# Optimization experiments

Hardware: AMD Instinct MI355X
Metric: run time of the kernel (lower is better)

The kernel has to match this reference:

```python
import jax, jax.numpy as jnp
import numpy as np

E, H, I = 5, 768, 1024  # num_experts, hidden_dim, intermediate_dim
TOP_K = 2


def setup_inputs() -> dict:
    key = jax.random.key(0)
    ks = jax.random.split(key, 6)
    s = 0.02
    return {
        "x": jax.random.normal(ks[0], (4, 2048, H), dtype=jnp.float32),
        "router_w": jax.random.normal(ks[1], (E, H), dtype=jnp.float32) * s,  # torch Linear (out,in)
        "router_b": jnp.zeros((E,), dtype=jnp.float32),
        "gate_w": jax.random.normal(ks[2], (E, H, I), dtype=jnp.float32) * s,
        "up_w": jax.random.normal(ks[3], (E, H, I), dtype=jnp.float32) * s,
        "down_w": jax.random.normal(ks[4], (E, I, H), dtype=jnp.float32) * s,
    }


def reference(x, router_w, router_b, gate_w, up_w, down_w):
    B, S, Hd = x.shape
    xf = x.reshape(-1, Hd)                       # [T, H]
    T = xf.shape[0]
    # Router: linear (with bias) -> softmax -> top-2 -> renormalize
    logits = xf @ router_w.T + router_b          # [T, E]
    scores = jax.nn.softmax(logits, axis=-1)
    vals, idx = jax.lax.top_k(scores, TOP_K)     # [T, 2]
    vals = vals / jnp.sum(vals, axis=-1, keepdims=True)
    # Dense combine weights: zero for unselected experts (same math as the
    # per-expert gather/scatter loop in the original module).
    comb = jnp.zeros((T, gate_w.shape[0]), dtype=x.dtype)
    comb = comb.at[jnp.arange(T)[:, None], idx].add(vals)  # [T, E]
    # SwiGLU per expert, vectorized over experts
    g = jnp.einsum('th,ehi->tei', xf, gate_w)    # [T, E, I]
    u = jnp.einsum('th,ehi->tei', xf, up_w)
    y = jnp.einsum('tei,eih->teh', jax.nn.silu(g) * u, down_w)  # [T, E, H]
    out = jnp.einsum('teh,te->th', y, comb)
    return out.reshape(B, S, Hd)
```

## Files before the change

kernel.cpp:

```cpp
#include <hip/hip_runtime.h>
#include <hip/hip_bf16.h>
#include <cstdint>
#include <cstddef>

#define T_TOK 8192
#define H_DIM 768
#define I_DIM 1024
#define N_EXP 5
#define MAXTILE 136

typedef short v8s __attribute__((ext_vector_type(8)));
typedef float v4f __attribute__((ext_vector_type(4)));

static __device__ __forceinline__ unsigned short f2bf(float f) {
    union { float f; unsigned int u; } v; v.f = f;
    unsigned int u = v.u;
    unsigned int r = (u + 0x7fffu + ((u >> 16) & 1u)) >> 16;
    return (unsigned short)r;
}
static __device__ __forceinline__ float bf2f(unsigned short s) {
    union { unsigned int u; float f; } v; v.u = ((unsigned int)s) << 16; return v.f;
}

static __device__ __forceinline__ void async16(const unsigned short* g, unsigned short* l) {
    __builtin_amdgcn_global_load_lds(
        (const __attribute__((address_space(1))) unsigned int*)g,
        (__attribute__((address_space(3))) unsigned int*)l, 16, 0, 0);
}

__global__ void k_prep(const float* __restrict__ gw, const float* __restrict__ uw,
                       const float* __restrict__ dw,
                       unsigned short* __restrict__ wbt, unsigned short* __restrict__ dbt,
                       const float* __restrict__ x, const float* __restrict__ rw,
                       const float* __restrict__ rb, unsigned short* __restrict__ xb,
                       int* __restrict__ top2e, float2* __restrict__ top2w) {
    const int z = blockIdx.z;
    const int tid = threadIdx.x;
    if (z < 3 * N_EXP) {
        __shared__ float tile[32][33];
        const int row = tid >> 3, cq = tid & 7;
        const int ocol = tid >> 3, seg = tid & 7;
        if (z < 2 * N_EXP) {
            if (blockIdx.y >= H_DIM / 32) return;
            const int e = z % N_EXP;
            const int isUp = z >= N_EXP;
            const float* src = (isUp ? uw : gw) + (size_t)e * H_DIM * I_DIM;
            const int c0 = blockIdx.x * 32, r0 = blockIdx.y * 32;
            float4 v = *(const float4*)(src + (size_t)(r0 + row) * I_DIM + c0 + cq * 4);
            tile[row][cq * 4 + 0] = v.x; tile[row][cq * 4 + 1] = v.y;
            tile[row][cq * 4 + 2] = v.z; tile[row][cq * 4 + 3] = v.w;
            __syncthreads();
            int c = c0 + ocol;
            int orow = (c >> 4) * 32 + (c & 15) + (isUp ? 16 : 0);
            ushort4 o;
            o.x = f2bf(tile[seg * 4 + 0][ocol]); o.y = f2bf(tile[seg * 4 + 1][ocol]);
            o.z = f2bf(tile[seg * 4 + 2][ocol]); o.w = f2bf(tile[seg * 4 + 3][ocol]);
            *(ushort4*)(wbt + ((size_t)e * 2 * I_DIM + orow) * H_DIM + r0 + seg * 4) = o;
        } else {
            if (blockIdx.x >= H_DIM / 32) return;
            const int e = z - 2 * N_EXP;
            const float* src = dw + (size_t)e * I_DIM * H_DIM;
            unsigned short* dst = dbt + (size_t)e * I_DIM * H_DIM;
            const int c0 = blockIdx.x * 32, r0 = blockIdx.y * 32;
            float4 v = *(const float4*)(src + (size_t)(r0 + row) * H_DIM + c0 + cq * 4);
            tile[row][cq * 4 + 0] = v.x; tile[row][cq * 4 + 1] = v.y;
            tile[row][cq * 4 + 2] = v.z; tile[row][cq * 4 + 3] = v.w;
            __syncthreads();
            ushort4 o;
            o.x = f2bf(tile[seg * 4 + 0][ocol]); o.y = f2bf(tile[seg * 4 + 1][ocol]);
            o.z = f2bf(tile[seg * 4 + 2][ocol]); o.w = f2bf(tile[seg * 4 + 3][ocol]);
            *(ushort4*)(dst + (size_t)(c0 + ocol) * I_DIM + r0 + seg * 4) = o;
        }
    } else {
        const int wave = tid >> 6, lane = tid & 63;
        const int t = (((z - 3 * N_EXP) * 1024 + blockIdx.y * 32 + blockIdx.x) * 4) + wave;
        const float* xr = x + (size_t)t * H_DIM;
        unsigned short* xbr = xb + (size_t)t * H_DIM;
        float acc[N_EXP];
#pragma unroll
        for (int e = 0; e < N_EXP; e++) acc[e] = 0.f;
#pragma unroll
        for (int j = 0; j < H_DIM / 256; j++) {
            int idx = j * 256 + lane * 4;
            float4 xv = *(const float4*)(xr + idx);
            ushort4 o;
            o.x = f2bf(xv.x); o.y = f2bf(xv.y); o.z = f2bf(xv.z); o.w = f2bf(xv.w);
            *(ushort4*)(xbr + idx) = o;
#pragma unroll
            for (int e = 0; e < N_EXP; e++) {
                float4 wv = *(const float4*)(rw + e * H_DIM + idx);
                acc[e] += xv.x * wv.x + xv.y * wv.y + xv.z * wv.z + xv.w * wv.w;
            }
        }
#pragma unroll
        for (int s = 32; s > 0; s >>= 1) {
#pragma unroll
            for (int e = 0; e < N_EXP; e++) acc[e] += __shfl_down(acc[e], s);
        }
        if (lane == 0) {
            float l[N_EXP];
#pragma unroll
            for (int e = 0; e < N_EXP; e++) l[e] = acc[e] + rb[e];
            int i1 = 0;
#pragma unroll
            for (int e = 1; e < N_EXP; e++) if (l[e] > l[i1]) i1 = e;
            int i2 = (i1 == 0) ? 1 : 0;
#pragma unroll
            for (int e = 0; e < N_EXP; e++) if (e != i1 && l[e] > l[i2]) i2 = e;
            float w1 = 1.f / (1.f + __expf(l[i2] - l[i1]));
            top2e[t] = i1 | (i2 << 8);
            top2w[t] = make_float2(w1, 1.f - w1);
        }
    }
}

__global__ void k_router_b(const int* __restrict__ top2e, const float2* __restrict__ top2w,
                           int* __restrict__ cnt, int* __restrict__ tokslot,
                           float* __restrict__ pweight, int* __restrict__ done,
                           int4* __restrict__ tiles) {
    __shared__ int lcnt[N_EXP], lbase[N_EXP];
    const int tid = threadIdx.x;
    if (tid < N_EXP) lcnt[tid] = 0;
    __syncthreads();
    const int t = blockIdx.x * 256 + tid;
    const int pe = top2e[t];
    const float2 wv = top2w[t];
    const int e1 = pe & 0xff, e2 = pe >> 8;
    const int s1 = atomicAdd(&lcnt[e1], 1);
    const int s2 = atomicAdd(&lcnt[e2], 1);
    __syncthreads();
    if (tid < N_EXP) lbase[tid] = atomicAdd(&cnt[tid], lcnt[tid]);
    __syncthreads();
    const int p1 = lbase[e1] + s1;
    tokslot[e1 * T_TOK + p1] = t; pweight[e1 * T_TOK + p1] = wv.x;
    const int p2 = lbase[e2] + s2;
    tokslot[e2 * T_TOK + p2] = t | (1 << 16); pweight[e2 * T_TOK + p2] = wv.y;
    __syncthreads();
    if (tid == 0) {
        __threadfence();
        if (atomicAdd(done, 1) == (int)gridDim.x - 1) {
            int c[N_EXP], off = 0, idx = 0;
            for (int e = 0; e < N_EXP; e++) c[e] = atomicAdd(&cnt[e], 0);
            for (int e = 0; e < N_EXP; e++) {
                for (int m0 = 0; m0 < c[e]; m0 += 128)
                    tiles[idx++] = make_int4(e, m0, off, c[e]);
                off += c[e];
            }
            for (; idx < MAXTILE; idx++) tiles[idx] = make_int4(-1, 0, 0, 0);
        }
    }
}

__launch_bounds__(256, 4)
__global__ void k_gateup(const unsigned short* __restrict__ xb,
                         const unsigned short* __restrict__ wbt,
                         const int4* __restrict__ tiles,
                         const int* __restrict__ tokslot,
                         const float* __restrict__ pweight,
                         unsigned short* __restrict__ hbuf) {
    const int4 td = tiles[blockIdx.x];
    const int e = td.x;
    if (e < 0) return;
    const int m0 = td.y, offe = td.z, cn = td.w;
    const int n0 = blockIdx.y * 64;

    __shared__ __align__(16) unsigned short ldsA[128 * 64];
    __shared__ __align__(16) unsigned short ldsB[128 * 64];

    const int tid = threadIdx.x;
    const int lane = tid & 63;
    const int wave = tid >> 6;
    const int fm = lane & 15, quad = lane >> 4;

    const int prow = lane >> 3;
    const int pc = lane & 7;
    const int lc8 = (pc ^ prow) * 8;

    unsigned aOff[4];
#pragma unroll
    for (int c = 0; c < 4; c++) {
        const int gr = m0 + c * 32 + wave * 8 + prow;
        const int tk = (gr < cn) ? (tokslot[e * T_TOK + gr] & 0xFFFF) : 0;
        aOff[c] = (unsigned)tk * H_DIM;
    }
    const unsigned short* aBase = xb + lc8;
    const unsigned short* bBase =
        wbt + ((size_t)e * 2 * I_DIM + n0 * 2 + wave * 8 + prow) * H_DIM + lc8;
    unsigned short* ldsAW = ldsA + wave * 8 * 64;
    unsigned short* ldsBW = ldsB + wave * 8 * 64;

    const int wm = (wave & 1) * 64, wnw = wave >> 1;

    v4f acc[4][4];
#pragma unroll
    for (int i = 0; i < 4; i++)
#pragma unroll
        for (int j = 0; j < 4; j++) acc[i][j] = (v4f)0.f;

    for (int kb = 0; kb < H_DIM / 64; kb++) {
        const int k0 = kb * 64;
#pragma unroll
        for (int c = 0; c < 4; c++)
            async16(aBase + aOff[c] + k0, ldsAW + c * 32 * 64);
#pragma unroll
        for (int c = 0; c < 4; c++)
            async16(bBase + (size_t)c * 32 * H_DIM + k0, ldsBW + c * 32 * 64);
        __syncthreads();
#pragma unroll
        for (int ks = 0; ks < 2; ks++) {
            const int pq = ((ks * 4 + quad) ^ (fm & 7)) * 8;
            v8s aF[4], bF[4];
#pragma unroll
            for (int im = 0; im < 4; im++)
                aF[im] = *(const v8s*)&ldsA[(wm + im * 16 + fm) * 64 + pq];
#pragma unroll
            for (int in = 0; in < 4; in++)
                bF[in] = *(const v8s*)&ldsB[(wnw * 64 + in * 16 + fm) * 64 + pq];
#pragma unroll
            for (int im = 0; im < 4; im++)
#pragma unroll
                for (int in = 0; in < 4; in++)
                    acc[im][in] = __builtin_amdgcn_mfma_f32_16x16x32_bf16(aF[im], bF[in], acc[im][in], 0, 0, 0);
        }
        __syncthreads();
    }

#pragma unroll
    for (int im = 0; im < 4; im++) {
        const int lr0 = wm + im * 16 + quad * 4;
        const float4 pw4 = *(const float4*)(pweight + e * T_TOK + m0 + lr0);
#pragma unroll
        for (int reg = 0; reg < 4; reg++) {
            int gr = m0 + lr0 + reg;
            if (gr < cn) {
                float pw = (&pw4.x)[reg];
                size_t base = (size_t)(offe + gr) * I_DIM + n0 + wnw * 32 + fm;
#pragma unroll
                for (int j = 0; j < 2; j++) {
                    float g = acc[im][2 * j][reg];
                    float u = acc[im][2 * j + 1][reg];
                    float s = g / (1.f + __expf(-g));
                    hbuf[base + j * 16] = f2bf(s * u * pw);
                }
            }
        }
    }
}

__launch_bounds__(256, 4)
__global__ void k_down(const unsigned short* __restrict__ hbuf,
                       const unsigned short* __restrict__ dbt,
                       const int4* __restrict__ tiles,
                       const int* __restrict__ tokslot,
                       unsigned short* __restrict__ ybuf) {
    const int4 td = tiles[blockIdx.x];
    const int e = td.x;
    if (e < 0) return;
    const int m0 = td.y, offe = td.z, cn = td.w;
    const int n0 = blockIdx.y * 128;

    __shared__ __align__(16) unsigned short ldsA[128 * 64];
    __shared__ __align__(16) unsigned short ldsB[128 * 64];

    const int tid = threadIdx.x;
    const int lane = tid & 63;
    const int wave = tid >> 6;
    const int fm = lane & 15, quad = lane >> 4;

    const int prow = lane >> 3;
    const int pc = lane & 7;
    const int lc8 = (pc ^ prow) * 8;

    unsigned aOff[4];
#pragma unroll
    for (int c = 0; c < 4; c++) {
        int ar = m0 + c * 32 + wave * 8 + prow;
        if (ar >= cn) ar = cn - 1;
        aOff[c] = (unsigned)(offe + ar) * I_DIM;
    }
    const unsigned short* aBase = hbuf + lc8;
    const unsigned short* bBase =
        dbt + ((size_t)e * H_DIM + n0 + wave * 8 + prow) * I_DIM + lc8;
    unsigned short* ldsAW = ldsA + wave * 8 * 64;
    unsigned short* ldsBW = ldsB + wave * 8 * 64;

    const int wm = (wave & 1) * 64, wn = (wave >> 1) * 64;

    v4f acc[4][4];
#pragma unroll
    for (int i = 0; i < 4; i++)
#pragma unroll
        for (int j = 0; j < 4; j++) acc[i][j] = (v4f)0.f;

    for (int kb = 0; kb < I_DIM / 64; kb++) {
        const int k0 = kb * 64;
#pragma unroll
        for (int c = 0; c < 4; c++)
            async16(aBase + aOff[c] + k0, ldsAW + c * 32 * 64);
#pragma unroll
        for (int c = 0; c < 4; c++)
            async16(bBase + (size_t)c * 32 * I_DIM + k0, ldsBW + c * 32 * 64);
        __syncthreads();
#pragma unroll
        for (int ks = 0; ks < 2; ks++) {
            const int pq = ((ks * 4 + quad) ^ (fm & 7)) * 8;
            v8s aF[4], bF[4];
#pragma unroll
            for (int im = 0; im < 4; im++)
                aF[im] = *(const v8s*)&ldsA[(wm + im * 16 + fm) * 64 + pq];
#pragma unroll
            for (int in = 0; in < 4; in++)
                bF[in] = *(const v8s*)&ldsB[(wn + in * 16 + fm) * 64 + pq];
#pragma unroll
            for (int im = 0; im < 4; im++)
#pragma unroll
                for (int in = 0; in < 4; in++)
                    acc[im][in] = __builtin_amdgcn_mfma_f32_16x16x32_bf16(aF[im], bF[in], acc[im][in], 0, 0, 0);
        }
        __syncthreads();
    }

#pragma unroll
    for (int im = 0; im < 4; im++) {
        const int lr0 = wm + im * 16 + quad * 4;
        const int4 tv4 = *(const int4*)(tokslot + e * T_TOK + m0 + lr0);
#pragma unroll
        for (int reg = 0; reg < 4; reg++) {
            int gr = m0 + lr0 + reg;
            if (gr < cn) {
                int v = (&tv4.x)[reg];
                int tok = v & 0xFFFF, s = (v >> 16) & 1;
#pragma unroll
                for (int in = 0; in < 4; in++) {
                    int col = n0 + wn + in * 16 + fm;
                    ybuf[((size_t)s * T_TOK + tok) * H_DIM + col] = f2bf(acc[im][in][reg]);
                }
            }
        }
    }
}

__global__ void k_combine(const unsigned short* __restrict__ ybuf, float* __restrict__ out) {
    const size_t i8 = ((size_t)blockIdx.x * 256 + threadIdx.x) * 8;
    const unsigned short* y0 = ybuf + i8;
    const unsigned short* y1 = ybuf + (size_t)T_TOK * H_DIM + i8;
    ushort4 a0 = *(const ushort4*)y0, a1 = *(const ushort4*)(y0 + 4);
    ushort4 b0 = *(const ushort4*)y1, b1 = *(const ushort4*)(y1 + 4);
    float4 o0, o1;
    o0.x = bf2f(a0.x) + bf2f(b0.x); o0.y = bf2f(a0.y) + bf2f(b0.y);
    o0.z = bf2f(a0.z) + bf2f(b0.z); o0.w = bf2f(a0.w) + bf2f(b0.w);
    o1.x = bf2f(a1.x) + bf2f(b1.x); o1.y = bf2f(a1.y) + bf2f(b1.y);
    o1.z = bf2f(a1.z) + bf2f(b1.z); o1.w = bf2f(a1.w) + bf2f(b1.w);
    *(float4*)(out + i8) = o0;
    *(float4*)(out + i8 + 4) = o1;
}

extern "C" void kernel_launch(void* const* d_in, const int* in_sizes, int n_in,
                              void* d_out, int out_size, void* d_ws, size_t ws_size,
                              hipStream_t stream) {
    const float* x  = (const float*)d_in[0];
    const float* rw = (const float*)d_in[1];
    const float* rb = (const float*)d_in[2];
    const float* gw = (const float*)d_in[3];
    const float* uw = (const float*)d_in[4];
    const float* dw = (const float*)d_in[5];
    float* out = (float*)d_out;

    char* ws = (char*)d_ws;
    size_t o = 0;
    auto alloc = [&](size_t bytes) { void* p = ws + o; o += (bytes + 255) & ~255ull; return p; };
    int*    cnt     = (int*)   alloc(8 * 4);
    int*    tokslot = (int*)   alloc((size_t)N_EXP * T_TOK * 4 + 512);
    float*  pweight = (float*) alloc((size_t)N_EXP * T_TOK * 4 + 512);
    int*    top2e   = (int*)   alloc((size_t)T_TOK * 4);
    float2* top2w   = (float2*)alloc((size_t)T_TOK * 8);
    int4*   tiles   = (int4*)  alloc((size_t)MAXTILE * 16);
    unsigned short* xb   = (unsigned short*)alloc((size_t)T_TOK * H_DIM * 2);
    unsigned short* wbt  = (unsigned short*)alloc((size_t)N_EXP * 2 * I_DIM * H_DIM * 2);
    unsigned short* dbt  = (unsigned short*)alloc((size_t)N_EXP * H_DIM * I_DIM * 2);
    unsigned short* hbuf = (unsigned short*)alloc((size_t)(2 * T_TOK + 128) * I_DIM * 2);
    unsigned short* ybuf = (unsigned short*)alloc((size_t)2 * T_TOK * H_DIM * 2);

    hipMemsetAsync(cnt, 0, 8 * 4, stream);

    dim3 pg(I_DIM / 32, I_DIM / 32, 3 * N_EXP + 2);
    k_prep<<<pg, 256, 0, stream>>>(gw, uw, dw, wbt, dbt, x, rw, rb, xb, top2e, top2w);

    k_router_b<<<T_TOK / 256, 256, 0, stream>>>(top2e, top2w, cnt, tokslot, pweight,
                                                cnt + 5, tiles);

    dim3 g1(MAXTILE, I_DIM / 64);
    k_gateup<<<g1, 256, 0, stream>>>(xb, wbt, tiles, tokslot, pweight, hbuf);

    dim3 g2(MAXTILE, H_DIM / 128);
    k_down<<<g2, 256, 0, stream>>>(hbuf, dbt, tiles, tokslot, ybuf);

    k_combine<<<(T_TOK * H_DIM) / (256 * 8), 256, 0, stream>>>(ybuf, out);
}
```

Baseline: 235.0 us.

## Fuse router slot assignment into prep kernel and halve GEMM N-tiles

Result: slower. 336.5 us (+43.2%).

```diff
diff --git a/kernel.cpp b/kernel.cpp
--- a/kernel.cpp
+++ b/kernel.cpp
@@ -8,6 +8,7 @@
 #define I_DIM 1024
 #define N_EXP 5
 #define MAXTILE 136
+#define NROUTER 2048
 
 typedef short v8s __attribute__((ext_vector_type(8)));
 typedef float v4f __attribute__((ext_vector_type(4)));
@@ -33,7 +34,9 @@
                        unsigned short* __restrict__ wbt, unsigned short* __restrict__ dbt,
                        const float* __restrict__ x, const float* __restrict__ rw,
                        const float* __restrict__ rb, unsigned short* __restrict__ xb,
-                       int* __restrict__ top2e, float2* __restrict__ top2w) {
+                       int* __restrict__ cnt, int* __restrict__ tokslot,
+                       float* __restrict__ pweight, int* __restrict__ done,
+                       int4* __restrict__ tiles) {
     const int z = blockIdx.z;
     const int tid = threadIdx.x;
     if (z < 3 * N_EXP) {
@@ -72,10 +75,12 @@
             *(ushort4*)(dst + (size_t)(c0 + ocol) * I_DIM + r0 + seg * 4) = o;
         }
     } else {
+        __shared__ int lcnt[N_EXP], lbase[N_EXP];
         const int wave = tid >> 6, lane = tid & 63;
         const int t = (((z - 3 * N_EXP) * 1024 + blockIdx.y * 32 + blockIdx.x) * 4) + wave;
         const float* xr = x + (size_t)t * H_DIM;
         unsigned short* xbr = xb + (size_t)t * H_DIM;
+        if (tid < N_EXP) lcnt[tid] = 0;
         float acc[N_EXP];
 #pragma unroll
         for (int e = 0; e < N_EXP; e++) acc[e] = 0.f;
@@ -97,56 +102,44 @@
 #pragma unroll
             for (int e = 0; e < N_EXP; e++) acc[e] += __shfl_down(acc[e], s);
         }
+        __syncthreads();
+        int i1 = 0, i2 = 0, s1 = 0, s2 = 0;
+        float w1 = 0.f;
         if (lane == 0) {
             float l[N_EXP];
 #pragma unroll
             for (int e = 0; e < N_EXP; e++) l[e] = acc[e] + rb[e];
-            int i1 = 0;
 #pragma unroll
             for (int e = 1; e < N_EXP; e++) if (l[e] > l[i1]) i1 = e;
-            int i2 = (i1 == 0) ? 1 : 0;
+            i2 = (i1 == 0) ? 1 : 0;
 #pragma unroll
             for (int e = 0; e < N_EXP; e++) if (e != i1 && l[e] > l[i2]) i2 = e;
-            float w1 = 1.f / (1.f + __expf(l[i2] - l[i1]));
-            top2e[t] = i1 | (i2 << 8);
-            top2w[t] = make_float2(w1, 1.f - w1);
-        }
-    }
-}
-
-__global__ void k_router_b(const int* __restrict__ top2e, const float2* __restrict__ top2w,
-                           int* __restrict__ cnt, int* __restrict__ tokslot,
-                           float* __restrict__ pweight, int* __restrict__ done,
-                           int4* __restrict__ tiles) {
-    __shared__ int lcnt[N_EXP], lbase[N_EXP];
-    const int tid = threadIdx.x;
-    if (tid < N_EXP) lcnt[tid] = 0;
-    __syncthreads();
-    const int t = blockIdx.x * 256 + tid;
-    const int pe = top2e[t];
-    const float2 wv = top2w[t];
-    const int e1 = pe & 0xff, e2 = pe >> 8;
-    const int s1 = atomicAdd(&lcnt[e1], 1);
-    const int s2 = atomicAdd(&lcnt[e2], 1);
-    __syncthreads();
-    if (tid < N_EXP) lbase[tid] = atomicAdd(&cnt[tid], lcnt[tid]);
-    __syncthreads();
-    const int p1 = lbase[e1] + s1;
-    tokslot[e1 * T_TOK + p1] = t; pweight[e1 * T_TOK + p1] = wv.x;
-    const int p2 = lbase[e2] + s2;
-    tokslot[e2 * T_TOK + p2] = t | (1 << 16); pweight[e2 * T_TOK + p2] = wv.y;
-    __syncthreads();
-    if (tid == 0) {
-        __threadfence();
-        if (atomicAdd(done, 1) == (int)gridDim.x - 1) {
-            int c[N_EXP], off = 0, idx = 0;
-            for (int e = 0; e < N_EXP; e++) c[e] = atomicAdd(&cnt[e], 0);
-            for (int e = 0; e < N_EXP; e++) {
-                for (int m0 = 0; m0 < c[e]; m0 += 128)
-                    tiles[idx++] = make_int4(e, m0, off, c[e]);
-                off += c[e];
+            w1 = 1.f / (1.f + __expf(l[i2] - l[i1]));
+            s1 = atomicAdd(&lcnt[i1], 1);
+            s2 = atomicAdd(&lcnt[i2], 1);
+        }
+        __syncthreads();
+        if (tid < N_EXP) lbase[tid] = atomicAdd(&cnt[tid], lcnt[tid]);
+        __syncthreads();
+        if (lane == 0) {
+            const int p1 = lbase[i1] + s1;
+            tokslot[i1 * T_TOK + p1] = t;            pweight[i1 * T_TOK + p1] = w1;
+            const int p2 = lbase[i2] + s2;
+            tokslot[i2 * T_TOK + p2] = t | (1 << 16); pweight[i2 * T_TOK + p2] = 1.f - w1;
+        }
+        __syncthreads();
+        if (tid == 0) {
+            __threadfence();
+            if (atomicAdd(done, 1) == NROUTER - 1) {
+                int c[N_EXP], off = 0, idx = 0;
+                for (int e = 0; e < N_EXP; e++) c[e] = atomicAdd(&cnt[e], 0);
+                for (int e = 0; e < N_EXP; e++) {
+                    for (int m0 = 0; m0 < c[e]; m0 += 128)
+                        tiles[idx++] = make_int4(e, m0, off, c[e]);
+                    off += c[e];
+                }
+                for (; idx < MAXTILE; idx++) tiles[idx] = make_int4(-1, 0, 0, 0);
             }
-            for (; idx < MAXTILE; idx++) tiles[idx] = make_int4(-1, 0, 0, 0);
         }
     }
 }
@@ -162,10 +155,10 @@
     const int e = td.x;
     if (e < 0) return;
     const int m0 = td.y, offe = td.z, cn = td.w;
-    const int n0 = blockIdx.y * 64;
+    const int n0 = blockIdx.y * 32;
 
     __shared__ __align__(16) unsigned short ldsA[128 * 64];
-    __shared__ __align__(16) unsigned short ldsB[128 * 64];
+    __shared__ __align__(16) unsigned short ldsB[64 * 64];
 
     const int tid = threadIdx.x;
     const int lane = tid & 63;
@@ -191,11 +184,11 @@
 
     const int wm = (wave & 1) * 64, wnw = wave >> 1;
 
-    v4f acc[4][4];
+    v4f acc[4][2];
 #pragma unroll
     for (int i = 0; i < 4; i++)
 #pragma unroll
-        for (int j = 0; j < 4; j++) acc[i][j] = (v4f)0.f;
+        for (int j = 0; j < 2; j++) acc[i][j] = (v4f)0.f;
 
     for (int kb = 0; kb < H_DIM / 64; kb++) {
         const int k0 = kb * 64;
@@ -203,23 +196,23 @@
         for (int c = 0; c < 4; c++)
             async16(aBase + aOff[c] + k0, ldsAW + c * 32 * 64);
 #pragma unroll
-        for (int c = 0; c < 4; c++)
+        for (int c = 0; c < 2; c++)
             async16(bBase + (size_t)c * 32 * H_DIM + k0, ldsBW + c * 32 * 64);
         __syncthreads();
 #pragma unroll
         for (int ks = 0; ks < 2; ks++) {
             const int pq = ((ks * 4 + quad) ^ (fm & 7)) * 8;
-            v8s aF[4], bF[4];
+            v8s aF[4], bF[2];
 #pragma unroll
             for (int im = 0; im < 4; im++)
                 aF[im] = *(const v8s*)&ldsA[(wm + im * 16 + fm) * 64 + pq];
 #pragma unroll
-            for (int in = 0; in < 4; in++)
-                bF[in] = *(const v8s*)&ldsB[(wnw * 64 + in * 16 + fm) * 64 + pq];
+            for (int in = 0; in < 2; in++)
+                bF[in] = *(const v8s*)&ldsB[(wnw * 32 + in * 16 + fm) * 64 + pq];
 #pragma unroll
             for (int im = 0; im < 4; im++)
 #pragma unroll
-                for (int in = 0; in < 4; in++)
+                for (int in = 0; in < 2; in++)
                     acc[im][in] = __builtin_amdgcn_mfma_f32_16x16x32_bf16(aF[im], bF[in], acc[im][in], 0, 0, 0);
         }
         __syncthreads();
@@ -234,14 +227,10 @@
             int gr = m0 + lr0 + reg;
             if (gr < cn) {
                 float pw = (&pw4.x)[reg];
-                size_t base = (size_t)(offe + gr) * I_DIM + n0 + wnw * 32 + fm;
-#pragma unroll
-                for (int j = 0; j < 2; j++) {
-                    float g = acc[im][2 * j][reg];
-                    float u = acc[im][2 * j + 1][reg];
-                    float s = g / (1.f + __expf(-g));
-                    hbuf[base + j * 16] = f2bf(s * u * pw);
-                }
+                float g = acc[im][0][reg];
+                float u = acc[im][1][reg];
+                float s = g / (1.f + __expf(-g));
+                hbuf[(size_t)(offe + gr) * I_DIM + n0 + wnw * 16 + fm] = f2bf(s * u * pw);
             }
         }
     }
@@ -257,10 +246,10 @@
     const int e = td.x;
     if (e < 0) return;
     const int m0 = td.y, offe = td.z, cn = td.w;
-    const int n0 = blockIdx.y * 128;
+    const int n0 = blockIdx.y * 64;
 
     __shared__ __align__(16) unsigned short ldsA[128 * 64];
-    __shared__ __align__(16) unsigned short ldsB[128 * 64];
+    __shared__ __align__(16) unsigned short ldsB[64 * 64];
 
     const int tid = threadIdx.x;
     const int lane = tid & 63;
@@ -284,13 +273,13 @@
     unsigned short* ldsAW = ldsA + wave * 8 * 64;
     unsigned short* ldsBW = ldsB + wave * 8 * 64;
 
-    const int wm = (wave & 1) * 64, wn = (wave >> 1) * 64;
-
-    v4f acc[4][4];
+    const int wm = (wave & 1) * 64, wnq = wave >> 1;
+
+    v4f acc[4][2];
 #pragma unroll
     for (int i = 0; i < 4; i++)
 #pragma unroll
-        for (int j = 0; j < 4; j++) acc[i][j] = (v4f)0.f;
+        for (int j = 0; j < 2; j++) acc[i][j] = (v4f)0.f;
 
     for (int kb = 0; kb < I_DIM / 64; kb++) {
         const int k0 = kb * 64;
@@ -298,23 +287,23 @@
         for (int c = 0; c < 4; c++)
             async16(aBase + aOff[c] + k0, ldsAW + c * 32 * 64);
 #pragma unroll
-        for (int c = 0; c < 4; c++)
+        for (int c = 0; c < 2; c++)
             async16(bBase + (size_t)c * 32 * I_DIM + k0, ldsBW + c * 32 * 64);
         __syncthreads();
 #pragma unroll
         for (int ks = 0; ks < 2; ks++) {
             const int pq = ((ks * 4 + quad) ^ (fm & 7)) * 8;
-            v8s aF[4], bF[4];
+            v8s aF[4], bF[2];
 #pragma unroll
             for (int im = 0; im < 4; im++)
                 aF[im] = *(const v8s*)&ldsA[(wm + im * 16 + fm) * 64 + pq];
 #pragma unroll
-            for (int in = 0; in < 4; in++)
-                bF[in] = *(const v8s*)&ldsB[(wn + in * 16 + fm) * 64 + pq];
+            for (int in = 0; in < 2; in++)
+                bF[in] = *(const v8s*)&ldsB[(wnq * 32 + in * 16 + fm) * 64 + pq];
 #pragma unroll
             for (int im = 0; im < 4; im++)
 #pragma unroll
-                for (int in = 0; in < 4; in++)
+                for (int in = 0; in < 2; in++)
                     acc[im][in] = __builtin_amdgcn_mfma_f32_16x16x32_bf16(aF[im], bF[in], acc[im][in], 0, 0, 0);
         }
         __syncthreads();
@@ -331,8 +320,8 @@
                 int v = (&tv4.x)[reg];
                 int tok = v & 0xFFFF, s = (v >> 16) & 1;
 #pragma unroll
-                for (int in = 0; in < 4; in++) {
-                    int col = n0 + wn + in * 16 + fm;
+                for (int in = 0; in < 2; in++) {
+                    int col = n0 + wnq * 32 + in * 16 + fm;
                     ybuf[((size_t)s * T_TOK + tok) * H_DIM + col] = f2bf(acc[im][in][reg]);
                 }
             }
@@ -372,8 +361,6 @@
     int*    cnt     = (int*)   alloc(8 * 4);
     int*    tokslot = (int*)   alloc((size_t)N_EXP * T_TOK * 4 + 512);
     float*  pweight = (float*) alloc((size_t)N_EXP * T_TOK * 4 + 512);
-    int*    top2e   = (int*)   alloc((size_t)T_TOK * 4);
-    float2* top2w   = (float2*)alloc((size_t)T_TOK * 8);
     int4*   tiles   = (int4*)  alloc((size_t)MAXTILE * 16);
     unsigned short* xb   = (unsigned short*)alloc((size_t)T_TOK * H_DIM * 2);
     unsigned short* wbt  = (unsigned short*)alloc((size_t)N_EXP * 2 * I_DIM * H_DIM * 2);
@@ -384,15 +371,13 @@
     hipMemsetAsync(cnt, 0, 8 * 4, stream);
 
     dim3 pg(I_DIM / 32, I_DIM / 32, 3 * N_EXP + 2);
-    k_prep<<<pg, 256, 0, stream>>>(gw, uw, dw, wbt, dbt, x, rw, rb, xb, top2e, top2w);
-
-    k_router_b<<<T_TOK / 256, 256, 0, stream>>>(top2e, top2w, cnt, tokslot, pweight,
-                                                cnt + 5, tiles);
-
-    dim3 g1(MAXTILE, I_DIM / 64);
+    k_prep<<<pg, 256, 0, stream>>>(gw, uw, dw, wbt, dbt, x, rw, rb, xb,
+                                   cnt, tokslot, pweight, cnt + 5, tiles);
+
+    dim3 g1(MAXTILE, I_DIM / 32);
     k_gateup<<<g1, 256, 0, stream>>>(xb, wbt, tiles, tokslot, pweight, hbuf);
 
-    dim3 g2(MAXTILE, H_DIM / 128);
+    dim3 g2(MAXTILE, H_DIM / 64);
     k_down<<<g2, 256, 0, stream>>>(hbuf, dbt, tiles, tokslot, ybuf);
 
     k_combine<<<(T_TOK * H_DIM) / (256 * 8), 256, 0, stream>>>(ybuf, out);
```
